# Performance work log

Measured on AMD Instinct MI355X. Metric: run time of the kernel, lower is better.

The kernel has to match this reference:

```python
import jax, jax.numpy as jnp
import numpy as np

N = 40000   # nodes
E = 640000  # edges (avg degree 16)
D = 128     # feature dim (in_features == out_features)
ALPHA = 0.2 # LeakyReLU negative slope


def setup_inputs() -> dict:
    key = jax.random.key(0)
    ks = jax.random.split(key, 12)
    s = 1.0 / np.sqrt(D)
    return {
        "h":     jax.random.normal(ks[0], (N, D), jnp.float32),
        "src":   jax.random.randint(ks[1], (E,), 0, N, jnp.int32),
        "dst":   jax.random.randint(ks[2], (E,), 0, N, jnp.int32),
        "W":     jax.random.normal(ks[3], (D, D), jnp.float32) * s,
        "b_W":   jnp.zeros((D,), jnp.float32),
        "a_src": jax.random.normal(ks[4], (D,), jnp.float32) * s,
        "a_dst": jax.random.normal(ks[5], (D,), jnp.float32) * s,
        "a_b":   jnp.zeros((1,), jnp.float32),
        "res_W": jax.random.normal(ks[6], (D, D), jnp.float32) * s,
        "res_b": jnp.zeros((D,), jnp.float32),
        "Wi":    jax.random.normal(ks[7], (3 * D, D), jnp.float32) * s,
        "Wh_g":  jax.random.normal(ks[8], (3 * D, D), jnp.float32) * s,
        "bi":    jnp.zeros((3 * D,), jnp.float32),
        "bh":    jnp.zeros((3 * D,), jnp.float32),
    }


def reference(h, src, dst, W, b_W, a_src, a_dst, a_b, res_W, res_b, Wi, Wh_g, bi, bh):
    # --- GAT layer: Wh = W h ---
    Wh = h @ W.T + b_W                                  # [N, D]
    # edge attention: a([Wh_src || Wh_dst]) == Wh_src@a_src + Wh_dst@a_dst + a_b
    s_s = Wh @ a_src                                    # [N]
    s_d = Wh @ a_dst                                    # [N]
    e = jax.nn.leaky_relu(s_s[src] + s_d[dst] + a_b[0], ALPHA)  # [E]
    # segment softmax over incoming edges of each destination node
    m = jax.ops.segment_max(e, dst, num_segments=N)
    m = jnp.where(jnp.isfinite(m), m, 0.0)
    ex = jnp.exp(e - m[dst])                            # [E]
    denom = jax.ops.segment_sum(ex, dst, num_segments=N)
    attn = ex / jnp.where(denom > 0, denom, 1.0)[dst]   # [E]
    # weighted neighbor aggregation (scatter-add on dst)
    h_prime = jax.ops.segment_sum(attn[:, None] * Wh[src], dst, num_segments=N)  # [N, D]
    # residual connection (res=True)
    h_prime = h_prime + h @ res_W.T + res_b
    # --- GRU cell: input = h_prime, hidden = h ---
    gi = h_prime @ Wi.T + bi                            # [N, 3D]
    gh = h @ Wh_g.T + bh                                # [N, 3D]
    i_r, i_z, i_n = jnp.split(gi, 3, axis=-1)
    h_r, h_z, h_n = jnp.split(gh, 3, axis=-1)
    r = jax.nn.sigmoid(i_r + h_r)
    z = jax.nn.sigmoid(i_z + h_z)
    n = jnp.tanh(i_n + r * h_n)
    return (1.0 - z) * n + z * h                        # [N, D]
```

## Files before the change

### kernel.cpp

```cpp
#include <hip/hip_runtime.h>
#include <math.h>

#define NLALPHA 0.2f
#define LOG2E 1.4426950408889634f
#define RT 10

typedef __attribute__((ext_vector_type(8))) short bf16x8;
typedef __attribute__((ext_vector_type(4))) float f32x4;

static __device__ __forceinline__ float fexp(float x) {
    return __builtin_amdgcn_exp2f(x * LOG2E);
}
static __device__ __forceinline__ float fsigmoid(float x) {
    return __builtin_amdgcn_rcpf(1.f + __builtin_amdgcn_exp2f(-LOG2E * x));
}
static __device__ __forceinline__ float ftanh(float x) {
    return 1.f - 2.f * __builtin_amdgcn_rcpf(1.f + __builtin_amdgcn_exp2f(2.f * LOG2E * x));
}
static __device__ __forceinline__ unsigned short f2bf(float f) {
    unsigned int u = __float_as_uint(f);
    return (unsigned short)((u + 0x7fffu + ((u >> 16) & 1u)) >> 16);
}
static __device__ __forceinline__ float bf2f(unsigned short b) {
    return __uint_as_float(((unsigned int)b) << 16);
}

__global__ __launch_bounds__(256) void k_zero(int* __restrict__ hist,
    float* __restrict__ s_s, float* __restrict__ s_d, int* __restrict__ counter, int n)
{
    int i = blockIdx.x * 256 + threadIdx.x;
    if (i < n) { hist[i] = 0; s_s[i] = 0.f; s_d[i] = 0.f; }
    if (i == 0) counter[0] = 0;
}

__global__ __launch_bounds__(256) void k_prep_hist(const float* __restrict__ h,
    const float* __restrict__ W, const float* __restrict__ res_W,
    const float* __restrict__ b_W, const float* __restrict__ res_b,
    const float* __restrict__ Wi, const float* __restrict__ Whg,
    const int* __restrict__ dstv,
    unsigned short* __restrict__ h_bf, unsigned short* __restrict__ Wcat,
    unsigned short* __restrict__ Wi_bf, unsigned short* __restrict__ Whg_bf,
    float* __restrict__ bias_cat, int* __restrict__ hist,
    int n, int e, int gPrep)
{
    const int b = blockIdx.x;
    if (b < gPrep) {
        int i = b * 256 + threadIdx.x;
        if (i < n * 16) {
            float4 v0 = ((const float4*)h)[2 * i];
            float4 v1 = ((const float4*)h)[2 * i + 1];
            uint4 o;
            o.x = (unsigned int)f2bf(v0.x) | ((unsigned int)f2bf(v0.y) << 16);
            o.y = (unsigned int)f2bf(v0.z) | ((unsigned int)f2bf(v0.w) << 16);
            o.z = (unsigned int)f2bf(v1.x) | ((unsigned int)f2bf(v1.y) << 16);
            o.w = (unsigned int)f2bf(v1.z) | ((unsigned int)f2bf(v1.w) << 16);
            ((uint4*)h_bf)[i] = o;
        }
        if (i < 32768) Wcat[i] = f2bf(i < 16384 ? W[i] : res_W[i - 16384]);
        if (i < 49152) { Wi_bf[i] = f2bf(Wi[i]); Whg_bf[i] = f2bf(Whg[i]); }
        if (i < 256) bias_cat[i] = (i < 128) ? b_W[i] : res_b[i - 128];
    } else {
        int i = (b - gPrep) * 256 + threadIdx.x;
        if (i < e) atomicAdd(&hist[dstv[i]], 1);
    }
}

__global__ __launch_bounds__(256) void k_alloc(const int* __restrict__ hist,
    int* __restrict__ counter, int* __restrict__ row_start, int* __restrict__ cursor, int n)
{
    int i = blockIdx.x * 256 + threadIdx.x;
    int lane = threadIdx.x & 63;
    int cnt = (i < n) ? hist[i] : 0;
    int inc = cnt;
#pragma unroll
    for (int o = 1; o < 64; o <<= 1) {
        int v = __shfl_up(inc, o);
        if (lane >= o) inc += v;
    }
    int total = __shfl(inc, 63);
    int base = 0;
    if (lane == 63) base = atomicAdd(counter, total);
    base = __shfl(base, 63);
    int ex = base + inc - cnt;
    if (i < n) { row_start[i] = ex; cursor[i] = ex; }
}

__global__ __launch_bounds__(256, 1) void k_whres_place(
    const unsigned short* __restrict__ h_bf,
    const unsigned short* __restrict__ Wcat, const float* __restrict__ bias_cat,
    const float* __restrict__ a_src, const float* __restrict__ a_dst,
    unsigned short* __restrict__ Wh, unsigned short* __restrict__ hres,
    float* __restrict__ s_s, float* __restrict__ s_d,
    const int* __restrict__ dstv, const int* __restrict__ srcv,
    int* __restrict__ cursor, int* __restrict__ esrc,
    int n, int e, int rowBlocks, int gWhres)
{
    const int b = blockIdx.x;
    if (b >= gWhres) {
        int i = (b - gWhres) * 256 + threadIdx.x;
        if (i < e) {
            int p = atomicAdd(&cursor[dstv[i]], 1);
            esrc[p] = srcv[i];
        }
        return;
    }
    const int bx = b % rowBlocks;
    const int by = b / rowBlocks;
    const int t = threadIdx.x;
    const int w = t >> 6, l = t & 63;
    const int lr = l & 15, kq = l >> 4, kg = kq * 8;
    const int jc = by * 64 + w * 16 + lr;
    bf16x8 bw[4];
#pragma unroll
    for (int ks = 0; ks < 4; ++ks)
        bw[ks] = *(const bf16x8*)(Wcat + (size_t)jc * 128 + ks * 32 + kg);
    const float bj = bias_cat[jc];
    const bool isWh = jc < 128;
    unsigned short* dstBase = isWh ? (Wh + jc) : (hres + (jc - 128));
    const float asj = isWh ? a_src[jc] : 0.f;
    const float adj = isWh ? a_dst[jc] : 0.f;

    int row0 = bx * (16 * RT);
    bf16x8 ac[4];
    {
        const unsigned short* Ap = h_bf + (size_t)min(row0 + lr, n - 1) * 128 + kg;
#pragma unroll
        for (int ks = 0; ks < 4; ++ks) ac[ks] = *(const bf16x8*)(Ap + ks * 32);
    }
    for (int rt = 0; rt < RT && row0 < n; ++rt) {
        const int nrow = row0 + 16;
        bf16x8 an[4];
        if (rt + 1 < RT && nrow < n) {
            const unsigned short* Ap = h_bf + (size_t)min(nrow + lr, n - 1) * 128 + kg;
#pragma unroll
            for (int ks = 0; ks < 4; ++ks) an[ks] = *(const bf16x8*)(Ap + ks * 32);
        }
        f32x4 acc = {};
        acc = __builtin_amdgcn_mfma_f32_16x16x32_bf16(ac[0], bw[0], acc, 0, 0, 0);
        acc = __builtin_amdgcn_mfma_f32_16x16x32_bf16(ac[1], bw[1], acc, 0, 0, 0);
        acc = __builtin_amdgcn_mfma_f32_16x16x32_bf16(ac[2], bw[2], acc, 0, 0, 0);
        acc = __builtin_amdgcn_mfma_f32_16x16x32_bf16(ac[3], bw[3], acc, 0, 0, 0);
#pragma unroll
        for (int r = 0; r < 4; ++r) {
            int row = row0 + kq * 4 + r;
            float v = acc[r] + bj;
            if (row < n) dstBase[(size_t)row * 128] = f2bf(v);
            if (isWh) {
                float ps = v * asj, pd = v * adj;
#pragma unroll
                for (int o = 1; o < 16; o <<= 1) {
                    ps += __shfl_xor(ps, o);
                    pd += __shfl_xor(pd, o);
                }
                if (lr == 0 && row < n) {
                    atomicAdd(&s_s[row], ps);
                    atomicAdd(&s_d[row], pd);
                }
            }
        }
#pragma unroll
        for (int ks = 0; ks < 4; ++ks) ac[ks] = an[ks];
        row0 = nrow;
    }
}

__global__ __launch_bounds__(256) void k_attn(const int* __restrict__ row_start,
    const int* __restrict__ hist, const int* __restrict__ esrc,
    const float* __restrict__ s_s, const float* __restrict__ s_d,
    const float* __restrict__ a_b, const unsigned short* __restrict__ Wh,
    const unsigned short* __restrict__ hres, unsigned short* __restrict__ hp, int n)
{
    const int node = (int)((blockIdx.x * 256u + threadIdx.x) >> 6);
    const int l = threadIdx.x & 63;
    if (node >= n) return;
    const int lo = row_start[node];
    const int cnt = hist[node];
    const int hi = lo + cnt;
    const float sdn = s_d[node] + a_b[0];
    const int g = l >> 4;
    const int c = l & 15;

    float sv = 0.f;
    int ssrc = 0;
    float den = 0.f;
    for (int p = lo + l; p < hi; p += 64) {
        int s = esrc[p];
        float ev = s_s[s] + sdn;
        ev = ev > 0.f ? ev : NLALPHA * ev;
        float ex = fexp(ev);
        if (p - lo < 64) { sv = ex; ssrc = s; }
        den += ex;
    }
#pragma unroll
    for (int o = 32; o; o >>= 1) den += __shfl_xor(den, o);
    const float dinv = __builtin_amdgcn_rcpf(den > 0.f ? den : 1.f);

    float acc[8] = {};
    const int q1 = min(cnt, 64);
    for (int q = 0; q < q1; q += 4) {
        int eix = q + g;
        bool valid = eix < cnt;
        int eic = valid ? eix : (cnt - 1);
        float ex = __shfl(sv, eic);
        int s = __shfl(ssrc, eic);
        float wgt = valid ? ex * dinv : 0.f;
        uint4 v = *(const uint4*)(Wh + (size_t)s * 128 + c * 8);
        acc[0] = fmaf(wgt, bf2f((unsigned short)(v.x & 0xffff)), acc[0]);
        acc[1] = fmaf(wgt, bf2f((unsigned short)(v.x >> 16)), acc[1]);
        acc[2] = fmaf(wgt, bf2f((unsigned short)(v.y & 0xffff)), acc[2]);
        acc[3] = fmaf(wgt, bf2f((unsigned short)(v.y >> 16)), acc[3]);
        acc[4] = fmaf(wgt, bf2f((unsigned short)(v.z & 0xffff)), acc[4]);
        acc[5] = fmaf(wgt, bf2f((unsigned short)(v.z >> 16)), acc[5]);
        acc[6] = fmaf(wgt, bf2f((unsigned short)(v.w & 0xffff)), acc[6]);
        acc[7] = fmaf(wgt, bf2f((unsigned short)(v.w >> 16)), acc[7]);
    }
    for (int q = 64; q < cnt; q += 4) {
        int eix = q + g;
        bool valid = eix < cnt;
        int eic = valid ? eix : (cnt - 1);
        int s = esrc[lo + eic];
        float ev = s_s[s] + sdn;
        ev = ev > 0.f ? ev : NLALPHA * ev;
        float wgt = valid ? fexp(ev) * dinv : 0.f;
        uint4 v = *(const uint4*)(Wh + (size_t)s * 128 + c * 8);
        acc[0] = fmaf(wgt, bf2f((unsigned short)(v.x & 0xffff)), acc[0]);
        acc[1] = fmaf(wgt, bf2f((unsigned short)(v.x >> 16)), acc[1]);
        acc[2] = fmaf(wgt, bf2f((unsigned short)(v.y & 0xffff)), acc[2]);
        acc[3] = fmaf(wgt, bf2f((unsigned short)(v.y >> 16)), acc[3]);
        acc[4] = fmaf(wgt, bf2f((unsigned short)(v.z & 0xffff)), acc[4]);
        acc[5] = fmaf(wgt, bf2f((unsigned short)(v.z >> 16)), acc[5]);
        acc[6] = fmaf(wgt, bf2f((unsigned short)(v.w & 0xffff)), acc[6]);
        acc[7] = fmaf(wgt, bf2f((unsigned short)(v.w >> 16)), acc[7]);
    }
#pragma unroll
    for (int k = 0; k < 8; ++k) {
        acc[k] += __shfl_xor(acc[k], 16);
        acc[k] += __shfl_xor(acc[k], 32);
    }
    if (l < 16) {
        uint4 hv = *(const uint4*)(hres + (size_t)node * 128 + l * 8);
        uint4 o;
        o.x = (unsigned int)f2bf(acc[0] + bf2f((unsigned short)(hv.x & 0xffff)))
            | ((unsigned int)f2bf(acc[1] + bf2f((unsigned short)(hv.x >> 16))) << 16);
        o.y = (unsigned int)f2bf(acc[2] + bf2f((unsigned short)(hv.y & 0xffff)))
            | ((unsigned int)f2bf(acc[3] + bf2f((unsigned short)(hv.y >> 16))) << 16);
        o.z = (unsigned int)f2bf(acc[4] + bf2f((unsigned short)(hv.z & 0xffff)))
            | ((unsigned int)f2bf(acc[5] + bf2f((unsigned short)(hv.z >> 16))) << 16);
        o.w = (unsigned int)f2bf(acc[6] + bf2f((unsigned short)(hv.w & 0xffff)))
            | ((unsigned int)f2bf(acc[7] + bf2f((unsigned short)(hv.w >> 16))) << 16);
        *(uint4*)(hp + (size_t)node * 128 + l * 8) = o;
    }
}

__global__ __launch_bounds__(256, 1) void k_gru(const unsigned short* __restrict__ hp_bf,
    const unsigned short* __restrict__ h_bf, const unsigned short* __restrict__ Wi_bf,
    const unsigned short* __restrict__ Whg_bf, const float* __restrict__ bi,
    const float* __restrict__ bh, float* __restrict__ out, int n)
{
    const int t = threadIdx.x;
    const int w = t >> 6, l = t & 63;
    const int lr = l & 15, kq = l >> 4, kg = kq * 8;
    const int c = blockIdx.y * 64 + w * 16 + lr;

    bf16x8 bwi[3][4], bwh[3][4];
#pragma unroll
    for (int g = 0; g < 3; ++g)
#pragma unroll
        for (int ks = 0; ks < 4; ++ks) {
            bwi[g][ks] = *(const bf16x8*)(Wi_bf  + (size_t)(g * 128 + c) * 128 + ks * 32 + kg);
            bwh[g][ks] = *(const bf16x8*)(Whg_bf + (size_t)(g * 128 + c) * 128 + ks * 32 + kg);
        }
    const float biR = bi[c],       bhR = bh[c];
    const float biZ = bi[128 + c], bhZ = bh[128 + c];
    const float biN = bi[256 + c], bhN = bh[256 + c];

    int row0 = blockIdx.x * (16 * RT);
    bf16x8 aPc[4], aHc[4];
    float hvc[4];
    {
        size_t rbase = (size_t)min(row0 + lr, n - 1) * 128 + kg;
#pragma unroll
        for (int ks = 0; ks < 4; ++ks) {
            aPc[ks] = *(const bf16x8*)(hp_bf + rbase + ks * 32);
            aHc[ks] = *(const bf16x8*)(h_bf + rbase + ks * 32);
        }
#pragma unroll
        for (int r = 0; r < 4; ++r)
            hvc[r] = bf2f(h_bf[(size_t)min(row0 + kq * 4 + r, n - 1) * 128 + c]);
    }
    for (int rt = 0; rt < RT && row0 < n; ++rt) {
        const int nrow = row0 + 16;
        bf16x8 aPn[4], aHn[4];
        float hvn[4];
        if (rt + 1 < RT && nrow < n) {
            size_t rbase = (size_t)min(nrow + lr, n - 1) * 128 + kg;
#pragma unroll
            for (int ks = 0; ks < 4; ++ks) {
                aPn[ks] = *(const bf16x8*)(hp_bf + rbase + ks * 32);
                aHn[ks] = *(const bf16x8*)(h_bf + rbase + ks * 32);
            }
#pragma unroll
            for (int r = 0; r < 4; ++r)
                hvn[r] = bf2f(h_bf[(size_t)min(nrow + kq * 4 + r, n - 1) * 128 + c]);
        }

        f32x4 giR = {}, giZ = {}, giN = {}, ghR = {}, ghZ = {}, ghN = {};
#pragma unroll
        for (int ks = 0; ks < 4; ++ks) {
            giR = __builtin_amdgcn_mfma_f32_16x16x32_bf16(aPc[ks], bwi[0][ks], giR, 0, 0, 0);
            ghR = __builtin_amdgcn_mfma_f32_16x16x32_bf16(aHc[ks], bwh[0][ks], ghR, 0, 0, 0);
            giZ = __builtin_amdgcn_mfma_f32_16x16x32_bf16(aPc[ks], bwi[1][ks], giZ, 0, 0, 0);
            ghZ = __builtin_amdgcn_mfma_f32_16x16x32_bf16(aHc[ks], bwh[1][ks], ghZ, 0, 0, 0);
            giN = __builtin_amdgcn_mfma_f32_16x16x32_bf16(aPc[ks], bwi[2][ks], giN, 0, 0, 0);
            ghN = __builtin_amdgcn_mfma_f32_16x16x32_bf16(aHc[ks], bwh[2][ks], ghN, 0, 0, 0);
        }
#pragma unroll
        for (int r = 0; r < 4; ++r) {
            int row = row0 + kq * 4 + r;
            if (row < n) {
                float rg = fsigmoid(giR[r] + biR + ghR[r] + bhR);
                float zg = fsigmoid(giZ[r] + biZ + ghZ[r] + bhZ);
                float ng = ftanh(giN[r] + biN + rg * (ghN[r] + bhN));
                out[(size_t)row * 128 + c] = (1.f - zg) * ng + zg * hvc[r];
            }
        }
#pragma unroll
        for (int ks = 0; ks < 4; ++ks) { aPc[ks] = aPn[ks]; aHc[ks] = aHn[ks]; }
#pragma unroll
        for (int r = 0; r < 4; ++r) hvc[r] = hvn[r];
        row0 = nrow;
    }
}

extern "C" void kernel_launch(void* const* d_in, const int* in_sizes, int n_in,
                              void* d_out, int out_size, void* d_ws, size_t ws_size,
                              hipStream_t stream)
{
    const float* h     = (const float*)d_in[0];
    const int*   srcv  = (const int*)d_in[1];
    const int*   dstv  = (const int*)d_in[2];
    const float* W     = (const float*)d_in[3];
    const float* b_W   = (const float*)d_in[4];
    const float* a_src = (const float*)d_in[5];
    const float* a_dst = (const float*)d_in[6];
    const float* a_b   = (const float*)d_in[7];
    const float* res_W = (const float*)d_in[8];
    const float* res_b = (const float*)d_in[9];
    const float* Wi    = (const float*)d_in[10];
    const float* Whg   = (const float*)d_in[11];
    const float* bi    = (const float*)d_in[12];
    const float* bh    = (const float*)d_in[13];
    float* out = (float*)d_out;
    const int n = in_sizes[0] / 128;
    const int e = in_sizes[1];
    const int rowBlocks = (n + 16 * RT - 1) / (16 * RT);
    const int gPrep  = (n * 16 + 255) / 256;
    const int gHist  = (e + 255) / 256;
    const int gWhres = rowBlocks * 4;
    const int gPlace = (e + 255) / 256;

    char* p = (char*)d_ws;
    auto carve = [&](size_t bytes) -> char* {
        char* r = p;
        p += (bytes + 255) & ~(size_t)255;
        return r;
    };
    unsigned short* h_bf   = (unsigned short*)carve((size_t)n * 128 * 2);
    unsigned short* Wh     = (unsigned short*)carve((size_t)n * 128 * 2);
    unsigned short* hres   = (unsigned short*)carve((size_t)n * 128 * 2);
    unsigned short* hp_bf  = (unsigned short*)carve((size_t)n * 128 * 2);
    float* s_s             = (float*)carve((size_t)n * 4);
    float* s_d             = (float*)carve((size_t)n * 4);
    int*   hist            = (int*)carve((size_t)n * 4);
    int*   row_start       = (int*)carve((size_t)n * 4);
    int*   cursor          = (int*)carve((size_t)n * 4);
    int*   esrc            = (int*)carve((size_t)e * 4);
    int*   counter         = (int*)carve(4);
    unsigned short* Wcat   = (unsigned short*)carve(32768 * 2);
    unsigned short* Wi_bf  = (unsigned short*)carve(49152 * 2);
    unsigned short* Whg_bf = (unsigned short*)carve(49152 * 2);
    float* bias_cat        = (float*)carve(256 * 4);

    k_zero<<<(n + 255) / 256, 256, 0, stream>>>(hist, s_s, s_d, counter, n);
    k_prep_hist<<<gPrep + gHist, 256, 0, stream>>>(h, W, res_W, b_W, res_b, Wi, Whg, dstv,
                                    h_bf, Wcat, Wi_bf, Whg_bf, bias_cat, hist, n, e, gPrep);
    k_alloc<<<(n + 255) / 256, 256, 0, stream>>>(hist, counter, row_start, cursor, n);
    k_whres_place<<<gWhres + gPlace, 256, 0, stream>>>(h_bf, Wcat, bias_cat, a_src, a_dst,
                                    Wh, hres, s_s, s_d, dstv, srcv, cursor, esrc,
                                    n, e, rowBlocks, gWhres);
    k_attn<<<((size_t)n * 64 + 255) / 256, 256, 0, stream>>>(row_start, hist, esrc, s_s, s_d,
                                                             a_b, Wh, hres, hp_bf, n);
    k_gru<<<dim3(rowBlocks, 2), 256, 0, stream>>>(hp_bf, h_bf, Wi_bf, Whg_bf, bi, bh, out, n);
}
```

Measured before the change: 159.4 us.

## Fold attention vectors into W to compute scores from h without atomics

Precomputes va = W^T a_src and W^T a_dst, plus bias constants, in an extra block of the zero kernel. The attention scores s_s and s_d are then computed directly from fp32 h during the bf16 conversion pass, using plain stores. This removes the per-row float atomicAdds and shuffle reductions from the MFMA projection kernel and drops the zeroing of s_s/s_d. The scores now come from fp32 h rather than the bf16 Wh, which changes numerics slightly. The extra zero-kernel block does a serial 128-step loop per thread.

Result: no change. 157.3 us (-1.3%).

```diff
diff --git a/kernel.cpp b/kernel.cpp
--- a/kernel.cpp
+++ b/kernel.cpp
@@ -26,26 +26,58 @@
 }
 
 __global__ __launch_bounds__(256) void k_zero(int* __restrict__ hist,
-    float* __restrict__ s_s, float* __restrict__ s_d, int* __restrict__ counter, int n)
-{
-    int i = blockIdx.x * 256 + threadIdx.x;
-    if (i < n) { hist[i] = 0; s_s[i] = 0.f; s_d[i] = 0.f; }
-    if (i == 0) counter[0] = 0;
+    int* __restrict__ counter, const float* __restrict__ W,
+    const float* __restrict__ a_src, const float* __restrict__ a_dst,
+    const float* __restrict__ b_W, float* __restrict__ va, float* __restrict__ cc,
+    int n, int gZero)
+{
+    const int b = blockIdx.x;
+    if (b < gZero) {
+        int i = b * 256 + threadIdx.x;
+        if (i < n) hist[i] = 0;
+        if (i == 0) counter[0] = 0;
+        return;
+    }
+    const int k = threadIdx.x;
+    float cs = 0.f, cd = 0.f;
+    if (k < 128) {
+        float ss = 0.f, dd = 0.f;
+        for (int j = 0; j < 128; ++j) {
+            float w = W[j * 128 + k];
+            ss = fmaf(w, a_src[j], ss);
+            dd = fmaf(w, a_dst[j], dd);
+        }
+        va[k] = ss;
+        va[128 + k] = dd;
+        cs = b_W[k] * a_src[k];
+        cd = b_W[k] * a_dst[k];
+    }
+#pragma unroll
+    for (int o = 32; o; o >>= 1) { cs += __shfl_down(cs, o); cd += __shfl_down(cd, o); }
+    __shared__ float sh[8];
+    if ((k & 63) == 0) { sh[(k >> 6) * 2] = cs; sh[(k >> 6) * 2 + 1] = cd; }
+    __syncthreads();
+    if (k == 0) {
+        cc[0] = sh[0] + sh[2] + sh[4] + sh[6];
+        cc[1] = sh[1] + sh[3] + sh[5] + sh[7];
+    }
 }
 
 __global__ __launch_bounds__(256) void k_prep_hist(const float* __restrict__ h,
     const float* __restrict__ W, const float* __restrict__ res_W,
     const float* __restrict__ b_W, const float* __restrict__ res_b,
     const float* __restrict__ Wi, const float* __restrict__ Whg,
-    const int* __restrict__ dstv,
+    const int* __restrict__ dstv, const float* __restrict__ va,
+    const float* __restrict__ cc,
     unsigned short* __restrict__ h_bf, unsigned short* __restrict__ Wcat,
     unsigned short* __restrict__ Wi_bf, unsigned short* __restrict__ Whg_bf,
-    float* __restrict__ bias_cat, int* __restrict__ hist,
-    int n, int e, int gPrep)
+    float* __restrict__ bias_cat, float* __restrict__ s_s, float* __restrict__ s_d,
+    int* __restrict__ hist, int n, int e, int gPrep)
 {
     const int b = blockIdx.x;
     if (b < gPrep) {
         int i = b * 256 + threadIdx.x;
+        int t = threadIdx.x;
         if (i < n * 16) {
             float4 v0 = ((const float4*)h)[2 * i];
             float4 v1 = ((const float4*)h)[2 * i + 1];
@@ -55,6 +87,22 @@
             o.z = (unsigned int)f2bf(v1.x) | ((unsigned int)f2bf(v1.y) << 16);
             o.w = (unsigned int)f2bf(v1.z) | ((unsigned int)f2bf(v1.w) << 16);
             ((uint4*)h_bf)[i] = o;
+            const float* vs = va + (t & 15) * 8;
+            const float* vd = vs + 128;
+            float ps = v0.x*vs[0] + v0.y*vs[1] + v0.z*vs[2] + v0.w*vs[3]
+                     + v1.x*vs[4] + v1.y*vs[5] + v1.z*vs[6] + v1.w*vs[7];
+            float pd = v0.x*vd[0] + v0.y*vd[1] + v0.z*vd[2] + v0.w*vd[3]
+                     + v1.x*vd[4] + v1.y*vd[5] + v1.z*vd[6] + v1.w*vd[7];
+#pragma unroll
+            for (int o2 = 1; o2 < 16; o2 <<= 1) {
+                ps += __shfl_xor(ps, o2);
+                pd += __shfl_xor(pd, o2);
+            }
+            if ((t & 15) == 0) {
+                int row = i >> 4;
+                s_s[row] = ps + cc[0];
+                s_d[row] = pd + cc[1];
+            }
         }
         if (i < 32768) Wcat[i] = f2bf(i < 16384 ? W[i] : res_W[i - 16384]);
         if (i < 49152) { Wi_bf[i] = f2bf(Wi[i]); Whg_bf[i] = f2bf(Whg[i]); }
@@ -88,9 +136,7 @@
 __global__ __launch_bounds__(256, 1) void k_whres_place(
     const unsigned short* __restrict__ h_bf,
     const unsigned short* __restrict__ Wcat, const float* __restrict__ bias_cat,
-    const float* __restrict__ a_src, const float* __restrict__ a_dst,
     unsigned short* __restrict__ Wh, unsigned short* __restrict__ hres,
-    float* __restrict__ s_s, float* __restrict__ s_d,
     const int* __restrict__ dstv, const int* __restrict__ srcv,
     int* __restrict__ cursor, int* __restrict__ esrc,
     int n, int e, int rowBlocks, int gWhres)
@@ -115,10 +161,7 @@
     for (int ks = 0; ks < 4; ++ks)
         bw[ks] = *(const bf16x8*)(Wcat + (size_t)jc * 128 + ks * 32 + kg);
     const float bj = bias_cat[jc];
-    const bool isWh = jc < 128;
-    unsigned short* dstBase = isWh ? (Wh + jc) : (hres + (jc - 128));
-    const float asj = isWh ? a_src[jc] : 0.f;
-    const float adj = isWh ? a_dst[jc] : 0.f;
+    unsigned short* dstBase = (jc < 128) ? (Wh + jc) : (hres + (jc - 128));
 
     int row0 = bx * (16 * RT);
     bf16x8 ac[4];
@@ -143,20 +186,7 @@
 #pragma unroll
         for (int r = 0; r < 4; ++r) {
             int row = row0 + kq * 4 + r;
-            float v = acc[r] + bj;
-            if (row < n) dstBase[(size_t)row * 128] = f2bf(v);
-            if (isWh) {
-                float ps = v * asj, pd = v * adj;
-#pragma unroll
-                for (int o = 1; o < 16; o <<= 1) {
-                    ps += __shfl_xor(ps, o);
-                    pd += __shfl_xor(pd, o);
-                }
-                if (lr == 0 && row < n) {
-                    atomicAdd(&s_s[row], ps);
-                    atomicAdd(&s_d[row], pd);
-                }
-            }
+            if (row < n) dstBase[(size_t)row * 128] = f2bf(acc[r] + bj);
         }
 #pragma unroll
         for (int ks = 0; ks < 4; ++ks) ac[ks] = an[ks];
@@ -354,6 +384,7 @@
     const int n = in_sizes[0] / 128;
     const int e = in_sizes[1];
     const int rowBlocks = (n + 16 * RT - 1) / (16 * RT);
+    const int gZero  = (n + 255) / 256;
     const int gPrep  = (n * 16 + 255) / 256;
     const int gHist  = (e + 255) / 256;
     const int gWhres = rowBlocks * 4;
@@ -380,13 +411,16 @@
     unsigned short* Wi_bf  = (unsigned short*)carve(49152 * 2);
     unsigned short* Whg_bf = (unsigned short*)carve(49152 * 2);
     float* bias_cat        = (float*)carve(256 * 4);
-
-    k_zero<<<(n + 255) / 256, 256, 0, stream>>>(hist, s_s, s_d, counter, n);
+    float* va              = (float*)carve(256 * 4);
+    float* cc              = (float*)carve(2 * 4);
+
+    k_zero<<<gZero + 1, 256, 0, stream>>>(hist, counter, W, a_src, a_dst, b_W, va, cc, n, gZero);
     k_prep_hist<<<gPrep + gHist, 256, 0, stream>>>(h, W, res_W, b_W, res_b, Wi, Whg, dstv,
-                                    h_bf, Wcat, Wi_bf, Whg_bf, bias_cat, hist, n, e, gPrep);
+                                    va, cc, h_bf, Wcat, Wi_bf, Whg_bf, bias_cat,
+                                    s_s, s_d, hist, n, e, gPrep);
     k_alloc<<<(n + 255) / 256, 256, 0, stream>>>(hist, counter, row_start, cursor, n);
-    k_whres_place<<<gWhres + gPlace, 256, 0, stream>>>(h_bf, Wcat, bias_cat, a_src, a_dst,
-                                    Wh, hres, s_s, s_d, dstv, srcv, cursor, esrc,
+    k_whres_place<<<gWhres + gPlace, 256, 0, stream>>>(h_bf, Wcat, bias_cat,
+                                    Wh, hres, dstv, srcv, cursor, esrc,
                                     n, e, rowBlocks, gWhres);
     k_attn<<<((size_t)n * 64 + 255) / 256, 256, 0, stream>>>(row_start, hist, esrc, s_s, s_d,
                                                              a_b, Wh, hres, hp_bf, n);
```
